# Kernel optimization log

Hardware: AMD Instinct MI355X
Metric: run time of the kernel (lower is better)

Reference implementation:

```python
import jax, jax.numpy as jnp
import numpy as np
from jax import lax

B, T, C, F = 32, 128, 64, 64
K, KH, KW = 128, 3, 64  # filters, kernel height (over channels axis), kernel width (= F -> F'=1)
BN_EPS = 1e-3  # keras BatchNormalization default epsilon


def setup_inputs() -> dict:
    key = jax.random.key(0)
    k1, k2 = jax.random.split(key)
    return {
        "x": jax.random.normal(k1, (B, T, C, F), dtype=jnp.float32),
        "conv_w": jax.random.normal(k2, (KH, KW, 1, K), dtype=jnp.float32) * 0.05,
        "conv_b": jnp.zeros((K,), dtype=jnp.float32),
        "bn_gamma": jnp.ones((T,), dtype=jnp.float32),
        "bn_beta": jnp.zeros((T,), dtype=jnp.float32),
        "bn_mean": jnp.zeros((T,), dtype=jnp.float32),
        "bn_var": jnp.ones((T,), dtype=jnp.float32),
    }


def reference(x, conv_w, conv_b, bn_gamma, bn_beta, bn_mean, bn_var):
    # Original loops Conv2D over each time step; we fold T into batch -> one conv.
    b, t, c, f = x.shape
    xr = x.reshape(b * t, c, f, 1)  # NHWC, spatial = (channels, features), 1 in-channel
    y = lax.conv_general_dilated(
        xr, conv_w, window_strides=(1, 1), padding="VALID",
        dimension_numbers=("NHWC", "HWIO", "NHWC"))
    y = y + conv_b  # (B*T, C'=c-KH+1, F'=1, K)
    cp = y.shape[1]
    y = y.reshape(b, t, cp, K)  # F'==1 squeezed; equals concat(axis=-1)+transposes in original
    # Dropout is identity at inference. BatchNorm (inference) over last axis of the
    # concatenated tensor (B, C', K, T) -> params indexed by T here.
    scale = (bn_gamma / jnp.sqrt(bn_var + BN_EPS))[None, :, None, None]
    shift = (bn_beta - bn_mean * bn_gamma / jnp.sqrt(bn_var + BN_EPS))[None, :, None, None]
    y = y * scale + shift
    y = jax.nn.relu(y)
    return y  # (B, T, C', K) -- matches original final transpose [0,3,1,2]
```

## Files before the change

### kernel.cpp

```cpp
#include <hip/hip_runtime.h>
#include <hip/hip_bf16.h>

#define NB   32
#define NT   128
#define NC   64
#define NF   64
#define NK   128
#define NCP  62
#define BN_EPS 1e-3f

typedef __attribute__((ext_vector_type(8))) short short8;
typedef __attribute__((ext_vector_type(4))) float floatx4;

__device__ __forceinline__ short f2bf(float f) {
    __hip_bfloat16 h = __float2bfloat16(f);
    return *reinterpret_cast<short*>(&h);
}

__global__ __launch_bounds__(256) void build_bfrag(
    const float* __restrict__ w, short8* __restrict__ bfrag)
{
    int idx  = blockIdx.x * 256 + threadIdx.x;
    int lane = idx & 63;
    int ts   = idx >> 6;
    int nt   = ts / 6;
    int s    = ts - nt * 6;
    int col  = lane & 15, q = lane >> 4;
    int n    = nt * 16 + col;
    int j0   = s * 32 + q * 8;
    short8 p;
    #pragma unroll
    for (int e = 0; e < 8; ++e) p[e] = f2bf(w[(size_t)(j0 + e) * NK + n]);
    bfrag[idx] = p;
}

__global__ __launch_bounds__(256, 4) void tccnn_mfma2(
    const float* __restrict__ x, const short8* __restrict__ bfrag,
    const float* __restrict__ bias, const float* __restrict__ gamma,
    const float* __restrict__ beta, const float* __restrict__ mean,
    const float* __restrict__ var, float* __restrict__ out)
{
    const int bt   = blockIdx.x;
    const int tid  = threadIdx.x;
    const int wv   = tid >> 6;
    const int lane = tid & 63;
    const int col  = lane & 15;
    const int q    = lane >> 4;
    const int t    = bt & (NT - 1);
    const int row  = wv * 16 + col;

    const float4* xg = (const float4*)x;
    const long maxi  = (long)NB * NT * 1024 - 2;
    long base4 = (long)bt * 1024 + row * 16 + q * 2;
    short8 afrag[6];
    #pragma unroll
    for (int s = 0; s < 6; ++s) {
        long i0 = base4 + s * 8;
        i0 = i0 > maxi ? maxi : i0;
        float4 v0 = xg[i0];
        float4 v1 = xg[i0 + 1];
        short8 p;
        p[0] = f2bf(v0.x); p[1] = f2bf(v0.y); p[2] = f2bf(v0.z); p[3] = f2bf(v0.w);
        p[4] = f2bf(v1.x); p[5] = f2bf(v1.y); p[6] = f2bf(v1.z); p[7] = f2bf(v1.w);
        afrag[s] = p;
    }

    floatx4 acc[8];
    #pragma unroll
    for (int nt = 0; nt < 8; ++nt) acc[nt] = (floatx4){0.f, 0.f, 0.f, 0.f};

    #pragma unroll
    for (int nt = 0; nt < 8; ++nt) {
        short8 b[6];
        #pragma unroll
        for (int s = 0; s < 6; ++s) b[s] = bfrag[(nt * 6 + s) * 64 + lane];
        #pragma unroll
        for (int s = 0; s < 6; ++s)
            acc[nt] = __builtin_amdgcn_mfma_f32_16x16x32_bf16(afrag[s], b[s], acc[nt], 0, 0, 0);
    }

    const float scale = gamma[t] * rsqrtf(var[t] + BN_EPS);
    const float shift = beta[t] - mean[t] * scale;

    float* obase = out + (size_t)bt * (NCP * NK);
    #pragma unroll
    for (int nt = 0; nt < 8; ++nt) {
        const int k  = nt * 16 + col;
        const float bv = bias[k];
        #pragma unroll
        for (int reg = 0; reg < 4; ++reg) {
            const int cp = wv * 16 + q * 4 + reg;
            if (cp < NCP) {
                float v = (acc[nt][reg] + bv) * scale + shift;
                obase[(size_t)cp * NK + k] = v > 0.f ? v : 0.f;
            }
        }
    }
}

extern "C" void kernel_launch(void* const* d_in, const int* in_sizes, int n_in,
                              void* d_out, int out_size, void* d_ws, size_t ws_size,
                              hipStream_t stream) {
    const float* x     = (const float*)d_in[0];
    const float* w     = (const float*)d_in[1];
    const float* bias  = (const float*)d_in[2];
    const float* gamma = (const float*)d_in[3];
    const float* beta  = (const float*)d_in[4];
    const float* mean  = (const float*)d_in[5];
    const float* var   = (const float*)d_in[6];
    float* out = (float*)d_out;
    short8* bfrag = (short8*)d_ws;

    build_bfrag<<<dim3(12), dim3(256), 0, stream>>>(w, bfrag);
    tccnn_mfma2<<<dim3(NB * NT), dim3(256), 0, stream>>>(
        x, bfrag, bias, gamma, beta, mean, var, out);
}
```

Before: 226.0 us.

## Assign N tiles to waves and loop over multiple batch-time rows per block

Each block now processes eight batch-time slices with 512 threads; each wave owns one 16-wide output-channel tile and keeps its weight fragments in registers while looping over row tiles. The BatchNorm scale/shift is precomputed in the prep kernel. This removes the repeated per-wave weight-fragment loads, but every wave now reloads and reconverts the same input rows, and the output stores become 64-byte column segments per wave.

```diff
diff --git a/kernel.cpp b/kernel.cpp
--- a/kernel.cpp
+++ b/kernel.cpp
@@ -3,11 +3,10 @@
 
 #define NB   32
 #define NT   128
-#define NC   64
-#define NF   64
 #define NK   128
 #define NCP  62
 #define BN_EPS 1e-3f
+#define NBT  8
 
 typedef __attribute__((ext_vector_type(8))) short short8;
 typedef __attribute__((ext_vector_type(4))) float floatx4;
@@ -17,8 +16,11 @@
     return *reinterpret_cast<short*>(&h);
 }
 
-__global__ __launch_bounds__(256) void build_bfrag(
-    const float* __restrict__ w, short8* __restrict__ bfrag)
+__global__ __launch_bounds__(256) void prep(
+    const float* __restrict__ w, const float* __restrict__ gamma,
+    const float* __restrict__ beta, const float* __restrict__ mean,
+    const float* __restrict__ var, short8* __restrict__ bfrag,
+    float2* __restrict__ ss)
 {
     int idx  = blockIdx.x * 256 + threadIdx.x;
     int lane = idx & 63;
@@ -32,70 +34,72 @@
     #pragma unroll
     for (int e = 0; e < 8; ++e) p[e] = f2bf(w[(size_t)(j0 + e) * NK + n]);
     bfrag[idx] = p;
+    if (idx < NT) {
+        float sc = gamma[idx] * rsqrtf(var[idx] + BN_EPS);
+        ss[idx] = make_float2(sc, beta[idx] - mean[idx] * sc);
+    }
 }
 
-__global__ __launch_bounds__(256, 4) void tccnn_mfma2(
+__global__ __launch_bounds__(512, 4) void tccnn_mfma3(
     const float* __restrict__ x, const short8* __restrict__ bfrag,
-    const float* __restrict__ bias, const float* __restrict__ gamma,
-    const float* __restrict__ beta, const float* __restrict__ mean,
-    const float* __restrict__ var, float* __restrict__ out)
+    const float* __restrict__ bias, const float2* __restrict__ ss,
+    float* __restrict__ out)
 {
-    const int bt   = blockIdx.x;
     const int tid  = threadIdx.x;
     const int wv   = tid >> 6;
     const int lane = tid & 63;
     const int col  = lane & 15;
     const int q    = lane >> 4;
-    const int t    = bt & (NT - 1);
-    const int row  = wv * 16 + col;
+    const int bt0  = blockIdx.x * NBT;
 
-    const float4* xg = (const float4*)x;
-    const long maxi  = (long)NB * NT * 1024 - 2;
-    long base4 = (long)bt * 1024 + row * 16 + q * 2;
-    short8 afrag[6];
+    short8 b[6];
     #pragma unroll
-    for (int s = 0; s < 6; ++s) {
-        long i0 = base4 + s * 8;
-        i0 = i0 > maxi ? maxi : i0;
-        float4 v0 = xg[i0];
-        float4 v1 = xg[i0 + 1];
-        short8 p;
-        p[0] = f2bf(v0.x); p[1] = f2bf(v0.y); p[2] = f2bf(v0.z); p[3] = f2bf(v0.w);
-        p[4] = f2bf(v1.x); p[5] = f2bf(v1.y); p[6] = f2bf(v1.z); p[7] = f2bf(v1.w);
-        afrag[s] = p;
-    }
+    for (int s = 0; s < 6; ++s) b[s] = bfrag[(wv * 6 + s) * 64 + lane];
 
-    floatx4 acc[8];
-    #pragma unroll
-    for (int nt = 0; nt < 8; ++nt) acc[nt] = (floatx4){0.f, 0.f, 0.f, 0.f};
+    const float bv = bias[wv * 16 + col];
 
-    #pragma unroll
-    for (int nt = 0; nt < 8; ++nt) {
-        short8 b[6];
-        #pragma unroll
-        for (int s = 0; s < 6; ++s) b[s] = bfrag[(nt * 6 + s) * 64 + lane];
-        #pragma unroll
-        for (int s = 0; s < 6; ++s)
-            acc[nt] = __builtin_amdgcn_mfma_f32_16x16x32_bf16(afrag[s], b[s], acc[nt], 0, 0, 0);
-    }
+    const float4* xg  = (const float4*)x;
+    const long   maxi = (long)NB * NT * 256 * 4 / 4 * 4;
+    const long   maxi4 = (long)NB * NT * 1024 - 2;
 
-    const float scale = gamma[t] * rsqrtf(var[t] + BN_EPS);
-    const float shift = beta[t] - mean[t] * scale;
+    for (int i = 0; i < NBT; ++i) {
+        const int bt = bt0 + i;
+        const float2 sshift = ss[bt & (NT - 1)];
 
-    float* obase = out + (size_t)bt * (NCP * NK);
-    #pragma unroll
-    for (int nt = 0; nt < 8; ++nt) {
-        const int k  = nt * 16 + col;
-        const float bv = bias[k];
-        #pragma unroll
-        for (int reg = 0; reg < 4; ++reg) {
-            const int cp = wv * 16 + q * 4 + reg;
-            if (cp < NCP) {
-                float v = (acc[nt][reg] + bv) * scale + shift;
-                obase[(size_t)cp * NK + k] = v > 0.f ? v : 0.f;
+        #pragma unroll 2
+        for (int mt = 0; mt < 4; ++mt) {
+            const int row = mt * 16 + col;
+            long base4 = (long)bt * 1024 + row * 16 + q * 2;
+            short8 a[6];
+            #pragma unroll
+            for (int s = 0; s < 6; ++s) {
+                long i0 = base4 + s * 8;
+                i0 = i0 > maxi4 ? maxi4 : i0;
+                float4 v0 = xg[i0];
+                float4 v1 = xg[i0 + 1];
+                short8 p;
+                p[0] = f2bf(v0.x); p[1] = f2bf(v0.y); p[2] = f2bf(v0.z); p[3] = f2bf(v0.w);
+                p[4] = f2bf(v1.x); p[5] = f2bf(v1.y); p[6] = f2bf(v1.z); p[7] = f2bf(v1.w);
+                a[s] = p;
+            }
+
+            floatx4 acc = (floatx4){0.f, 0.f, 0.f, 0.f};
+            #pragma unroll
+            for (int s = 0; s < 6; ++s)
+                acc = __builtin_amdgcn_mfma_f32_16x16x32_bf16(a[s], b[s], acc, 0, 0, 0);
+
+            float* ob = out + (size_t)bt * (NCP * NK) + wv * 16 + col;
+            #pragma unroll
+            for (int reg = 0; reg < 4; ++reg) {
+                const int cp = mt * 16 + q * 4 + reg;
+                if (cp < NCP) {
+                    float v = (acc[reg] + bv) * sshift.x + sshift.y;
+                    ob[(size_t)cp * NK] = v > 0.f ? v : 0.f;
+                }
             }
         }
     }
+    (void)maxi;
 }
 
 extern "C" void kernel_launch(void* const* d_in, const int* in_sizes, int n_in,
@@ -109,9 +113,11 @@
     const float* mean  = (const float*)d_in[5];
     const float* var   = (const float*)d_in[6];
     float* out = (float*)d_out;
+
     short8* bfrag = (short8*)d_ws;
+    float2* ss    = (float2*)((char*)d_ws + 3072 * 16);
 
-    build_bfrag<<<dim3(12), dim3(256), 0, stream>>>(w, bfrag);
-    tccnn_mfma2<<<dim3(NB * NT), dim3(256), 0, stream>>>(
-        x, bfrag, bias, gamma, beta, mean, var, out);
+    prep<<<dim3(12), dim3(256), 0, stream>>>(w, gamma, beta, mean, var, bfrag, ss);
+    tccnn_mfma3<<<dim3(NB * NT / NBT), dim3(512), 0, stream>>>(
+        x, bfrag, bias, ss, out);
 }
```

Result: slower. 325.7 us (+44.1%).
